# Optimization experiments

Measured on AMD Instinct MI355X. Metric: run time of the kernel, lower is better.

The kernel has to match this reference:

```python
import jax, jax.numpy as jnp
import numpy as np
from jax import lax

H = 16        # linear_num_key_heads == linear_num_value_heads
DK = 64       # linear_key_head_dim
DV = 128      # linear_value_head_dim
HID = 2048    # hidden_size
KCONV = 4     # linear_conv_kernel_dim
SEQ = 2048
KEY_DIM = H * DK       # 1024
VAL_DIM = H * DV       # 2048
CONV_DIM = 2 * KEY_DIM + VAL_DIM  # 4096


def _l2norm(x, eps=1e-6):
    return x * lax.rsqrt(jnp.sum(x * x, axis=-1, keepdims=True) + eps)


def setup_inputs() -> dict:
    key = jax.random.key(0)
    ks = jax.random.split(key, 10)
    s = 0.02
    return {
        "hidden_states": jax.random.normal(ks[0], (1, SEQ, HID), jnp.float32),
        "in_proj_qkv": jax.random.normal(ks[1], (CONV_DIM, HID), jnp.float32) * s,
        "in_proj_a": jax.random.normal(ks[2], (H, HID), jnp.float32) * s,
        "in_proj_b": jax.random.normal(ks[3], (H, HID), jnp.float32) * s,
        "in_proj_z": jax.random.normal(ks[4], (VAL_DIM, HID), jnp.float32) * s,
        "conv_w": jax.random.normal(ks[5], (CONV_DIM, 1, KCONV), jnp.float32) * 0.5,
        "A_log": jax.random.normal(ks[6], (H,), jnp.float32) * 0.5,
        "dt_bias": jnp.ones((H,), jnp.float32),
        "norm_w": jnp.ones((DV,), jnp.float32),
        "out_proj": jax.random.normal(ks[7], (HID, VAL_DIM), jnp.float32) * s,
        "is_prefill": 1,
    }


def reference(hidden_states, in_proj_qkv, in_proj_a, in_proj_b, in_proj_z,
              conv_w, A_log, dt_bias, norm_w, out_proj, is_prefill):
    b, s, _ = hidden_states.shape  # b == 1
    # QKV projection: (1, S, CONV_DIM)
    mixed = jnp.einsum('bsh,oh->bso', hidden_states, in_proj_qkv)
    # Depthwise causal conv1d over time (left pad K-1), then SiLU
    x = mixed.transpose(0, 2, 1)  # (1, C, S)
    x = lax.conv_general_dilated(
        x, conv_w, window_strides=(1,), padding=[(KCONV - 1, 0)],
        feature_group_count=CONV_DIM, dimension_numbers=('NCH', 'OIH', 'NCH'))
    mixed = jax.nn.silu(x).transpose(0, 2, 1)[0]  # (S, CONV_DIM), squeeze batch

    q = mixed[:, :KEY_DIM].reshape(s, H, DK)
    k = mixed[:, KEY_DIM:2 * KEY_DIM].reshape(s, H, DK)
    v = mixed[:, 2 * KEY_DIM:].reshape(s, H, DV)

    hs = hidden_states[0]  # (S, HID)
    a = hs @ in_proj_a.T                      # (S, H)
    g = -jnp.exp(A_log) * jax.nn.softplus(a + dt_bias)  # (S, H) log-decay
    beta = jax.nn.sigmoid(hs @ in_proj_b.T)   # (S, H)
    z = (hs @ in_proj_z.T).reshape(s, H, DV)  # (S, H, DV)

    q = _l2norm(q) * (1.0 / np.sqrt(DK))
    k = _l2norm(k)

    # Delta-rule recurrence; prefill -> zero initial state
    S0 = jnp.zeros((H, DK, DV), jnp.float32)

    def step(St, inp):
        q_t, k_t, v_t, g_t, beta_t = inp
        St = St * jnp.exp(g_t)[:, None, None]            # decay
        kv_mem = jnp.einsum('hk,hkv->hv', k_t, St)       # read
        delta = (v_t - kv_mem) * beta_t[:, None]         # gated error
        St = St + jnp.einsum('hk,hv->hkv', k_t, delta)   # rank-1 update
        o_t = jnp.einsum('hk,hkv->hv', q_t, St)          # query read
        return St, o_t

    _, core = lax.scan(step, S0, (q, k, v, g, beta))  # core: (S, H, DV)

    # Gated RMSNorm over DV, then SiLU(z) gate
    var = jnp.mean(core * core, axis=-1, keepdims=True)
    core = core * lax.rsqrt(var + 1e-6) * norm_w
    core = core * jax.nn.silu(z)
    core = core.reshape(1, s, VAL_DIM)
    return jnp.einsum('bsv,hv->bsh', core, out_proj)
```

## Files before the change

### kernel.cpp

```cpp
#include <hip/hip_runtime.h>
#include <stdint.h>


#define SEQ 2048
#define HIDDEN 2048
#define NH 16
#define DKv 64
#define DVv 128
#define KEY_DIM 1024
#define VAL_DIM 2048
#define CONV_DIM 4096

typedef __bf16 bf16;
typedef unsigned short u16;
typedef __attribute__((ext_vector_type(8))) __bf16 bf16x8;
typedef __attribute__((ext_vector_type(4))) __bf16 bf16x4;
typedef __attribute__((ext_vector_type(4))) float f32x4;

#define AS1 __attribute__((address_space(1)))
#define AS3 __attribute__((address_space(3)))
#define GLDS16(src, dst) __builtin_amdgcn_global_load_lds((AS1 const void*)(src), (AS3 void*)(dst), 16, 0, 0)

__device__ __forceinline__ float b2f(u16 u) {
  union { unsigned int i; float f; } c; c.i = ((unsigned int)u) << 16; return c.f;
}
__device__ __forceinline__ float sigmoidf_(float x) { return 1.0f / (1.0f + __expf(-x)); }

__global__ void detect_dtype(const u16* __restrict__ p, unsigned* __restrict__ flag) {
  int lane = threadIdx.x;
  int cnt = 0;
  for (int w = lane; w < 2048; w += 64) {
    unsigned e = (p[2 * w] >> 7) & 0xFF;
    if (e < 64) cnt++;
  }
  cnt += __shfl_xor(cnt, 1);  cnt += __shfl_xor(cnt, 2);  cnt += __shfl_xor(cnt, 4);
  cnt += __shfl_xor(cnt, 8);  cnt += __shfl_xor(cnt, 16); cnt += __shfl_xor(cnt, 32);
  if (lane == 0) *flag = (cnt > 64) ? 1u : 0u;
}

__global__ __launch_bounds__(256)
void cvt_bf16(const void* __restrict__ src, bf16* __restrict__ dst, long n,
              const unsigned* __restrict__ flagp) {
  long i = ((long)blockIdx.x * 256 + threadIdx.x) * 8;
  if (i >= n) return;
  if (*flagp) {
    const f32x4* s = (const f32x4*)((const float*)src + i);
    f32x4 a = s[0], b = s[1];
    bf16x8 o;
#pragma unroll
    for (int j = 0; j < 4; ++j) { o[j] = (bf16)a[j]; o[4 + j] = (bf16)b[j]; }
    *(bf16x8*)(dst + i) = o;
  } else {
    *(bf16x8*)(dst + i) = *(const bf16x8*)((const bf16*)src + i);
  }
}

template<bool F32OUT>
__global__ __launch_bounds__(256, 2)
void gemm_nt(const void* __restrict__ Araw, const void* __restrict__ Braw,
             void* __restrict__ Cv, int N, int K,
             const unsigned* __restrict__ flagp, int useA, int useB) {
  __shared__ __align__(16) bf16 As[128 * 32];
  __shared__ __align__(16) bf16 Bs[128 * 32];
  const bool f32g = (*flagp != 0);
  const bool fA = useA && f32g;
  const bool fB = useB && f32g;
  const int tid  = threadIdx.x;
  const int lane = tid & 63;
  const int wv   = tid >> 6;
  const int wm   = (wv & 1) << 6;
  const int wn   = (wv >> 1) << 6;
  const long bm  = (long)blockIdx.y * 128;
  const long bn  = (long)blockIdx.x * 128;

  f32x4 acc[4][4] = {};

  for (int k0 = 0; k0 < K; k0 += 32) {
#pragma unroll
    for (int it = 0; it < 2; ++it) {
      int e   = (it * 256 + tid) * 8;
      int row = e >> 5;
      int col = e & 31;
      long offA = (bm + row) * (long)K + (k0 + col);
      long offB = (bn + row) * (long)K + (k0 + col);
      if (fA) {
        const float* g = (const float*)Araw + offA;
        f32x4 u0 = *(const f32x4*)g, u1 = *(const f32x4*)(g + 4);
        bf16x8 bv;
#pragma unroll
        for (int j = 0; j < 4; ++j) { bv[j] = (bf16)u0[j]; bv[4 + j] = (bf16)u1[j]; }
        *(bf16x8*)&As[e] = bv;
      } else {
        const bf16* g = (const bf16*)Araw + offA;
        GLDS16(g, &As[e]);
      }
      if (fB) {
        const float* g = (const float*)Braw + offB;
        f32x4 u0 = *(const f32x4*)g, u1 = *(const f32x4*)(g + 4);
        bf16x8 bv;
#pragma unroll
        for (int j = 0; j < 4; ++j) { bv[j] = (bf16)u0[j]; bv[4 + j] = (bf16)u1[j]; }
        *(bf16x8*)&Bs[e] = bv;
      } else {
        const bf16* g = (const bf16*)Braw + offB;
        GLDS16(g, &Bs[e]);
      }
    }
    __syncthreads();

    const bf16x8* As8 = (const bf16x8*)As;
    const bf16x8* Bs8 = (const bf16x8*)Bs;
    const int r = lane & 15, q = lane >> 4;
    bf16x8 af[4], bfr[4];
#pragma unroll
    for (int i = 0; i < 4; ++i) af[i]  = As8[(wm + i * 16 + r) * 4 + q];
#pragma unroll
    for (int j = 0; j < 4; ++j) bfr[j] = Bs8[(wn + j * 16 + r) * 4 + q];
#pragma unroll
    for (int i = 0; i < 4; ++i)
#pragma unroll
      for (int j = 0; j < 4; ++j)
        acc[i][j] = __builtin_amdgcn_mfma_f32_16x16x32_bf16(af[i], bfr[j], acc[i][j], 0, 0, 0);
    __syncthreads();
  }

  const int r = lane & 15, q = lane >> 4;
#pragma unroll
  for (int i = 0; i < 4; ++i)
#pragma unroll
    for (int j = 0; j < 4; ++j) {
      long row = bm + wm + i * 16 + q * 4;
      long col = bn + wn + j * 16 + r;
#pragma unroll
      for (int rr = 0; rr < 4; ++rr) {
        if constexpr (F32OUT) ((float*)Cv)[(row + rr) * N + col] = acc[i][j][rr];
        else                  ((bf16*)Cv)[(row + rr) * N + col] = (bf16)acc[i][j][rr];
      }
    }
}

__device__ void gemm_body_bf16(char* smemc, const bf16* __restrict__ A,
                               const bf16* __restrict__ B, bf16* __restrict__ C,
                               int N, int K, int bx, int by, int tid) {
  bf16* As = (bf16*)smemc;
  bf16* Bs = (bf16*)(smemc + 8192);
  const int lane = tid & 63;
  const int wv = tid >> 6, wm = (wv & 1) << 6, wn = (wv >> 1) << 6;
  const long bm = (long)by * 128, bn = (long)bx * 128;
  f32x4 acc[4][4] = {};
  for (int k0 = 0; k0 < K; k0 += 32) {
#pragma unroll
    for (int it = 0; it < 2; ++it) {
      int e = (it * 256 + tid) * 8;
      int row = e >> 5, col = e & 31;
      const bf16* gA = A + (bm + row) * (long)K + k0 + col;
      const bf16* gB = B + (bn + row) * (long)K + k0 + col;
      GLDS16(gA, &As[e]);
      GLDS16(gB, &Bs[e]);
    }
    __syncthreads();
    const bf16x8* As8 = (const bf16x8*)As;
    const bf16x8* Bs8 = (const bf16x8*)Bs;
    const int r = lane & 15, q = lane >> 4;
    bf16x8 af[4], bfr[4];
#pragma unroll
    for (int i = 0; i < 4; ++i) af[i]  = As8[(wm + i * 16 + r) * 4 + q];
#pragma unroll
    for (int j = 0; j < 4; ++j) bfr[j] = Bs8[(wn + j * 16 + r) * 4 + q];
#pragma unroll
    for (int i = 0; i < 4; ++i)
#pragma unroll
      for (int j = 0; j < 4; ++j)
        acc[i][j] = __builtin_amdgcn_mfma_f32_16x16x32_bf16(af[i], bfr[j], acc[i][j], 0, 0, 0);
    __syncthreads();
  }
  const int r = lane & 15, q = lane >> 4;
#pragma unroll
  for (int i = 0; i < 4; ++i)
#pragma unroll
    for (int j = 0; j < 4; ++j) {
      long row = bm + wm + i * 16 + q * 4;
      long col = bn + wn + j * 16 + r;
#pragma unroll
      for (int rr = 0; rr < 4; ++rr)
        C[(row + rr) * (long)N + col] = (bf16)acc[i][j][rr];
    }
}

__global__ __launch_bounds__(256)
void proj_ab(const void* __restrict__ hsr, const void* __restrict__ War,
             const void* __restrict__ Wbr, const void* __restrict__ A_logr,
             const void* __restrict__ dtbr,
             float* __restrict__ eg, float* __restrict__ bet,
             float* __restrict__ gb,
             const unsigned* __restrict__ flagp) {
  const bool f32g = (*flagp != 0);
  const int t  = threadIdx.x;
  const int sl = t >> 5;
  const int o  = t & 31;
  const int h  = o & 15;
  const long s = (long)blockIdx.x * 8 + sl;
  float a0 = 0.f, a1 = 0.f, a2 = 0.f, a3 = 0.f;
  if (f32g) {
    const f32x4* x4 = (const f32x4*)((const float*)hsr + s * HIDDEN);
    const f32x4* w4 = (const f32x4*)((const float*)((o < 16) ? War : Wbr) + (long)h * HIDDEN);
#pragma unroll 8
    for (int k4 = 0; k4 < 512; ++k4) {
      f32x4 xv = x4[k4], wv = w4[k4];
      a0 = fmaf(xv[0], wv[0], a0);
      a1 = fmaf(xv[1], wv[1], a1);
      a2 = fmaf(xv[2], wv[2], a2);
      a3 = fmaf(xv[3], wv[3], a3);
    }
  } else {
    const bf16x8* x8 = (const bf16x8*)((const bf16*)hsr + s * HIDDEN);
    const bf16x8* w8 = (const bf16x8*)((const bf16*)((o < 16) ? War : Wbr) + (long)h * HIDDEN);
#pragma unroll 8
    for (int k8 = 0; k8 < 256; ++k8) {
      bf16x8 xv = x8[k8], wv = w8[k8];
      a0 += (float)xv[0] * (float)wv[0] + (float)xv[4] * (float)wv[4];
      a1 += (float)xv[1] * (float)wv[1] + (float)xv[5] * (float)wv[5];
      a2 += (float)xv[2] * (float)wv[2] + (float)xv[6] * (float)wv[6];
      a3 += (float)xv[3] * (float)wv[3] + (float)xv[7] * (float)wv[7];
    }
  }
  const float a = (a0 + a1) + (a2 + a3);
  if (o < 16) {
    float alog = f32g ? ((const float*)A_logr)[h] : b2f(((const u16*)A_logr)[h]);
    float dtb  = f32g ? ((const float*)dtbr)[h]   : b2f(((const u16*)dtbr)[h]);
    float xx = a + dtb;
    float sp = fmaxf(xx, 0.f) + log1pf(__expf(-fabsf(xx)));
    float gg = -__expf(alog) * sp;
    if (gb) gb[s * NH + h] = gg;
    eg[s * NH + h] = __expf(gg);
  } else {
    bet[s * NH + h] = sigmoidf_(a);
  }
}

__global__ __launch_bounds__(256)
void conv_norm(const bf16* __restrict__ mixed, const void* __restrict__ convwr,
               bf16* __restrict__ qbuf, bf16* __restrict__ kbuf, bf16* __restrict__ vbuf,
               const unsigned* __restrict__ flagp) {
  const bool f32g = (*flagp != 0);
  const int s = blockIdx.x;
  const int c = blockIdx.y * 256 + threadIdx.x;
  float w0, w1, w2, w3;
  if (f32g) {
    const float* wp = (const float*)convwr + (long)c * 4;
    w0 = wp[0]; w1 = wp[1]; w2 = wp[2]; w3 = wp[3];
  } else {
    const u16* wp = (const u16*)convwr + (long)c * 4;
    w0 = b2f(wp[0]); w1 = b2f(wp[1]); w2 = b2f(wp[2]); w3 = b2f(wp[3]);
  }
  float acc = w3 * (float)mixed[(long)s * CONV_DIM + c];
  if (s >= 1) acc += w2 * (float)mixed[(long)(s - 1) * CONV_DIM + c];
  if (s >= 2) acc += w1 * (float)mixed[(long)(s - 2) * CONV_DIM + c];
  if (s >= 3) acc += w0 * (float)mixed[(long)(s - 3) * CONV_DIM + c];
  float y = acc * sigmoidf_(acc);
  if (c < 2 * KEY_DIM) {
    float ss = y * y;
    ss += __shfl_xor(ss, 1);  ss += __shfl_xor(ss, 2);  ss += __shfl_xor(ss, 4);
    ss += __shfl_xor(ss, 8);  ss += __shfl_xor(ss, 16); ss += __shfl_xor(ss, 32);
    float scale = rsqrtf(ss + 1e-6f);
    if (c < KEY_DIM) scale *= 0.125f;
    y *= scale;
  }
  if (c < KEY_DIM)            qbuf[(long)s * KEY_DIM + c] = (bf16)y;
  else if (c < 2 * KEY_DIM)   kbuf[(long)s * KEY_DIM + (c - KEY_DIM)] = (bf16)y;
  else                        vbuf[(long)s * VAL_DIM + (c - 2 * KEY_DIM)] = (bf16)y;
}

template<int CTRL>
__device__ __forceinline__ float dpp_add(float x) {
  int y = __builtin_amdgcn_update_dpp(0, __float_as_int(x), CTRL, 0xF, 0xF, true);
  return x + __int_as_float(y);
}
__device__ __forceinline__ float dpp_sum16(float x) {
  x = dpp_add<0xB1>(x);
  x = dpp_add<0x4E>(x);
  x = dpp_add<0x141>(x);
  x = dpp_add<0x140>(x);
  return x;
}

__global__ __launch_bounds__(256, 2)
void fused_scan(const bf16* __restrict__ qbuf, const bf16* __restrict__ kbuf,
                const bf16* __restrict__ vbuf, const float* __restrict__ eg,
                const float* __restrict__ bet, bf16* __restrict__ core,
                const bf16* __restrict__ hsb, const bf16* __restrict__ wzb,
                bf16* __restrict__ zbuf, const void* __restrict__ woutr,
                bf16* __restrict__ woutb, const unsigned* __restrict__ flagp,
                int nScan, int nGemm) {
  __shared__ __align__(16) char smem[16384];
  const int t = threadIdx.x;
  const int b = blockIdx.x;

  if (b < nScan) {
    const int h  = b >> 3;
    const int vg = (b & 7) * 16;
    const int g  = t >> 4;
    const int L  = t & 15;
    bf16*  kqs = (bf16*)smem;
    bf16*  vts = (bf16*)(smem + 8192);
    float* ets = (float*)(smem + 9216);
    float* bts = (float*)(smem + 9344);

#define STAGE(buf, s0)                                                          \
    {                                                                           \
      int byte = t * 16;                                                        \
      const bf16* src;                                                          \
      if (byte < 2048) {                                                        \
        int row = byte >> 7, el = (byte & 127) >> 1;                            \
        src = kbuf + (long)((s0) + row) * KEY_DIM + h * DKv + el;               \
      } else {                                                                  \
        int b2 = byte - 2048;                                                   \
        int row = b2 >> 7, el = (b2 & 127) >> 1;                                \
        src = qbuf + (long)((s0) + row) * KEY_DIM + h * DKv + el;               \
      }                                                                         \
      GLDS16(src, smem + (buf) * 4096 + byte);                                  \
      if (t < 32) {                                                             \
        int row = t >> 1, el = (t & 1) * 8;                                     \
        const bf16* vsrc = vbuf + (long)((s0) + row) * VAL_DIM + h * DVv + vg + el; \
        GLDS16(vsrc, smem + 8192 + (buf) * 512 + t * 16);                       \
      }                                                                         \
    }

    float er = 0.f, br = 0.f;
    if (t < 16)      er = eg[(long)t * NH + h];
    else if (t < 32) br = bet[(long)(t - 16) * NH + h];
    STAGE(0, 0);
    if (t < 16)      ets[t] = er;
    else if (t < 32) bts[t - 16] = br;
    __syncthreads();

    float S0 = 0.f, S1 = 0.f, S2 = 0.f, S3 = 0.f;
    for (int tile = 0; tile < 128; ++tile) {
      const int buf = tile & 1, nb = buf ^ 1;
      if (tile < 127) {
        STAGE(nb, (tile + 1) * 16);
        if (t < 16)      er = eg[(long)((tile + 1) * 16 + t) * NH + h];
        else if (t < 32) br = bet[(long)((tile + 1) * 16 + (t - 16)) * NH + h];
      }
      const bf16*  ktb = kqs + buf * 2048;
      const bf16*  qtb = ktb + 1024;
      const bf16*  vtb = vts + buf * 256;
      const float* etb = ets + buf * 16;
      const float* btb = bts + buf * 16;
      const long sbase = (long)tile * 16;

      bf16x4 kR[2], qR[2];
      float  vR[2], eR[2], bR[2];
      kR[0] = *(const bf16x4*)(ktb + 0 * 64 + L * 4);
      qR[0] = *(const bf16x4*)(qtb + 0 * 64 + L * 4);
      vR[0] = (float)vtb[0 * 16 + g];  eR[0] = etb[0];  bR[0] = btb[0];
      kR[1] = *(const bf16x4*)(ktb + 1 * 64 + L * 4);
      qR[1] = *(const bf16x4*)(qtb + 1 * 64 + L * 4);
      vR[1] = (float)vtb[1 * 16 + g];  eR[1] = etb[1];  bR[1] = btb[1];
#pragma unroll
      for (int s = 0; s < 16; ++s) {
        const int sl = s & 1;
        bf16x4 kk = kR[sl], qq = qR[sl];
        float vv = vR[sl], ee = eR[sl], bb = bR[sl];
        if (s < 14) {
          const int s2 = s + 2;
          kR[sl] = *(const bf16x4*)(ktb + s2 * 64 + L * 4);
          qR[sl] = *(const bf16x4*)(qtb + s2 * 64 + L * 4);
          vR[sl] = (float)vtb[s2 * 16 + g];
          eR[sl] = etb[s2];  bR[sl] = btb[s2];
        }
        float ebt = ee * bb, vbt = vv * bb;
        float k0 = (float)kk[0], k1 = (float)kk[1], k2 = (float)kk[2], k3 = (float)kk[3];
        float D0 = S0 * ee, D1 = S1 * ee, D2 = S2 * ee, D3 = S3 * ee;
        float p = (k0 * S0 + k1 * S1) + (k2 * S2 + k3 * S3);
        p = dpp_sum16(p);
        float delta = vbt - ebt * p;
        S0 = fmaf(k0, delta, D0); S1 = fmaf(k1, delta, D1);
        S2 = fmaf(k2, delta, D2); S3 = fmaf(k3, delta, D3);
        float q0 = (float)qq[0], q1 = (float)qq[1], q2 = (float)qq[2], q3 = (float)qq[3];
        float o = (q0 * S0 + q1 * S1) + (q2 * S2 + q3 * S3);
        o = dpp_sum16(o);
        if (L == 0) core[(sbase + s) * VAL_DIM + h * DVv + vg + g] = (bf16)o;
      }
      if (tile < 127) {
        if (t < 16)      ets[nb * 16 + t] = er;
        else if (t < 32) bts[nb * 16 + (t - 16)] = br;
      }
      __syncthreads();
    }
#undef STAGE
  } else if (b < nScan + nGemm) {
    int gb = b - nScan;
    gemm_body_bf16(smem, hsb, wzb, zbuf, VAL_DIM, HIDDEN, gb & 15, gb >> 4, t);
  } else {
    long i = ((long)(b - nScan - nGemm) * 256 + t) * 8;
    if (i < (long)HIDDEN * VAL_DIM) {
      if (*flagp) {
        const f32x4* s = (const f32x4*)((const float*)woutr + i);
        f32x4 a = s[0], c = s[1];
        bf16x8 o;
#pragma unroll
        for (int j = 0; j < 4; ++j) { o[j] = (bf16)a[j]; o[4 + j] = (bf16)c[j]; }
        *(bf16x8*)(woutb + i) = o;
      } else {
        *(bf16x8*)(woutb + i) = *(const bf16x8*)((const bf16*)woutr + i);
      }
    }
  }
}


__global__ __launch_bounds__(256, 2)
void chunk_a(const bf16* __restrict__ kbuf, const bf16* __restrict__ vbuf,
             const float* __restrict__ gbuf, const float* __restrict__ betp,
             bf16* __restrict__ dloc, bf16* __restrict__ whig, bf16* __restrict__ wlog,
             const bf16* __restrict__ hsb, const bf16* __restrict__ wzb,
             bf16* __restrict__ zbuf, const void* __restrict__ woutr,
             bf16* __restrict__ woutb, const unsigned* __restrict__ flagp) {
  __shared__ __align__(16) char smem[25600];
  const int t = threadIdx.x;
  const int b = blockIdx.x;
  if (b < 512) {
    const int c = b >> 4, h = b & 15;
    bf16*  Ks   = (bf16*)smem;
    float* At   = (float*)(smem + 8192);
    float* cumS = (float*)(smem + 24576);
    float* bS   = (float*)(smem + 24832);
    float* dS   = (float*)(smem + 25088);
#pragma unroll
    for (int it = 0; it < 2; ++it) {
      int byte = (it * 256 + t) * 16;
      int row = byte >> 7, col = (byte & 127) >> 1;
      const bf16* src = kbuf + (long)(c * 64 + row) * KEY_DIM + h * DKv + col;
      GLDS16(src, smem + byte);
    }
    if (t < 64) {
      float cc = gbuf[(long)(c * 64 + t) * NH + h];
#pragma unroll
      for (int d = 1; d < 64; d <<= 1) { float y = __shfl_up(cc, d); if (t >= d) cc += y; }
      cumS[t] = cc;
      dS[t] = __expf(cc);
      bS[t] = betp[(long)(c * 64 + t) * NH + h];
    }
    {
      f32x4 z = {0.f, 0.f, 0.f, 0.f};
#pragma unroll
      for (int i = 0; i < 4; ++i) ((f32x4*)At)[t * 4 + i] = z;
    }
    __syncthreads();
    {
      const int lane = t & 63, wv = t >> 6;
      const int r = lane & 15, q = lane >> 4;
      const bf16x8* Ks8 = (const bf16x8*)Ks;
#pragma unroll
      for (int n = 0; n < 4; ++n) {
        f32x4 acc = {0.f, 0.f, 0.f, 0.f};
#pragma unroll
        for (int kk = 0; kk < 2; ++kk) {
          bf16x8 af  = Ks8[(wv * 16 + r) * 8 + kk * 4 + q];
          bf16x8 bfv = Ks8[(n  * 16 + r) * 8 + kk * 4 + q];
          acc = __builtin_amdgcn_mfma_f32_16x16x32_bf16(af, bfv, acc, 0, 0, 0);
        }
        const int i = n * 16 + r;
#pragma unroll
        for (int rr = 0; rr < 4; ++rr) {
          const int tr = wv * 16 + q * 4 + rr;
          if (i < tr)
            At[i * 64 + tr] = bS[tr] * __expf(cumS[tr] - cumS[i]) * acc[rr];
        }
      }
    }
    __syncthreads();
    if (t < 192) {
      float x[64];
      const long base = ((long)(c * 16 + h)) * 64;
      if (t < 128) {
#pragma unroll
        for (int s = 0; s < 64; ++s)
          x[s] = bS[s] * (float)vbuf[(long)(c * 64 + s) * VAL_DIM + h * DVv + t];
      } else {
        const int k = t - 128;
#pragma unroll
        for (int s = 0; s < 64; ++s)
          x[s] = bS[s] * dS[s] * (float)Ks[s * 64 + k];
      }
#pragma unroll
      for (int s = 0; s < 64; ++s) {
        const float val = x[s];
        const f32x4* row4 = (const f32x4*)(At + s * 64);
#pragma unroll
        for (int qd = (s >> 2); qd < 16; ++qd) {
          f32x4 a4 = row4[qd];
          x[qd * 4 + 0] = fmaf(-a4[0], val, x[qd * 4 + 0]);
          x[qd * 4 + 1] = fmaf(-a4[1], val, x[qd * 4 + 1]);
          x[qd * 4 + 2] = fmaf(-a4[2], val, x[qd * 4 + 2]);
          x[qd * 4 + 3] = fmaf(-a4[3], val, x[qd * 4 + 3]);
        }
      }
      if (t < 128) {
#pragma unroll
        for (int s = 0; s < 64; ++s)
          dloc[(base + s) * 128 + t] = (bf16)x[s];
      } else {
        const int k = t - 128;
        const long wb = base * 64;
#pragma unroll
        for (int s = 0; s < 64; ++s) {
          float v = -x[s];
          bf16 hh = (bf16)v;
          whig[wb + s * 64 + k] = hh;
          wlog[wb + s * 64 + k] = (bf16)(v - (float)hh);
        }
      }
    }
  } else if (b < 768) {
    int gb = b - 512;
    gemm_body_bf16(smem, hsb, wzb, zbuf, VAL_DIM, HIDDEN, gb & 15, gb >> 4, t);
  } else {
    long i = ((long)(b - 768) * 256 + t) * 8;
    if (i < (long)HIDDEN * VAL_DIM) {
      if (*flagp) {
        const f32x4* s = (const f32x4*)((const float*)woutr + i);
        f32x4 a = s[0], cc = s[1];
        bf16x8 o;
#pragma unroll
        for (int j = 0; j < 4; ++j) { o[j] = (bf16)a[j]; o[4 + j] = (bf16)cc[j]; }
        *(bf16x8*)(woutb + i) = o;
      } else {
        *(bf16x8*)(woutb + i) = *(const bf16x8*)((const bf16*)woutr + i);
      }
    }
  }
}

__global__ __launch_bounds__(256, 1)
void chunk_b(const bf16* __restrict__ qbuf, const bf16* __restrict__ kbuf,
             const float* __restrict__ gbuf, const bf16* __restrict__ dloc,
             const bf16* __restrict__ whig, const bf16* __restrict__ wlog,
             bf16* __restrict__ dTg, bf16* __restrict__ o1g) {
  __shared__ __align__(16) char smem[139264];
  bf16* Wh  = (bf16*)(smem);
  bf16* Wl  = (bf16*)(smem + 16384);
  bf16* Qs  = (bf16*)(smem + 32768);
  bf16* Ks  = (bf16*)(smem + 49152);
  bf16* Dls = (bf16*)(smem + 65536);
  bf16* KT  = (bf16*)(smem + 81920);
  bf16* Shi = (bf16*)(smem + 90112);
  bf16* Slo = (bf16*)(smem + 98304);
  bf16* Dth = (bf16*)(smem + 106496);
  bf16* Dtl = (bf16*)(smem + 114688);
  float* fSa = (float*)(smem + 122880);
  float* dSa = (float*)(smem + 131072);

  const int t = threadIdx.x;
  const int h = blockIdx.x >> 1, vhalf = blockIdx.x & 1;
  const int lane = t & 63, w = t >> 6;
  const int r = lane & 15, q = lane >> 4;
  const int tb = w * 16 + q * 4;

  auto stage = [&](int bb, int cc) {
    const long c16h = (long)(cc * 16 + h);
#pragma unroll
    for (int it = 0; it < 2; ++it) {
      int p = it * 256 + t;
      int row = p >> 3, g = p & 7;
      int sg = ((g ^ (row & 7)) << 3);
      GLDS16(whig + c16h * 4096 + row * 64 + sg, (char*)Wh + bb * 8192 + p * 16);
      GLDS16(wlog + c16h * 4096 + row * 64 + sg, (char*)Wl + bb * 8192 + p * 16);
      GLDS16(qbuf + (long)(cc * 64 + row) * KEY_DIM + h * DKv + sg, (char*)Qs + bb * 8192 + p * 16);
      GLDS16(kbuf + (long)(cc * 64 + row) * KEY_DIM + h * DKv + (g << 3), (char*)Ks + bb * 8192 + p * 16);
      GLDS16(dloc + (c16h * 64 + row) * 128 + vhalf * 64 + sg, (char*)Dls + bb * 8192 + p * 16);
    }
  };

  {
    float g8[8];
#pragma unroll
    for (int i = 0; i < 8; ++i)
      g8[i] = gbuf[(long)((w * 8 + i) * 64 + lane) * NH + h];
#pragma unroll
    for (int i = 0; i < 8; ++i) {
      float cs = g8[i];
#pragma unroll
      for (int d = 1; d < 64; d <<= 1) { float y = __shfl_up(cs, d); if (lane >= d) cs += y; }
      float tot = __shfl(cs, 63);
      fSa[(w * 8 + i) * 64 + lane] = __expf(tot - cs);
      dSa[(w * 8 + i) * 64 + lane] = __expf(cs);
    }
  }
  {
    f32x4 z = {0.f, 0.f, 0.f, 0.f};
    ((f32x4*)Shi)[t] = z; ((f32x4*)Shi)[t + 256] = z;
    ((f32x4*)Slo)[t] = z; ((f32x4*)Slo)[t + 256] = z;
  }
  stage(0, 0);
  f32x4 Sacc[4] = {};

  for (int c = 0; c < 32; ++c) {
    const int buf = c & 1, nb = buf ^ 1;
    __syncthreads();
    if (c < 31) stage(nb, c + 1);
    const bf16* wh = Wh + buf * 4096;
    const bf16* wl = Wl + buf * 4096;
    const bf16* qs = Qs + buf * 4096;
    const bf16* ks = Ks + buf * 4096;
    const bf16* dl = Dls + buf * 4096;
    const float* fS = fSa + c * 64;
    const float* dS = dSa + c * 64;
    const long gch = (long)(c * 16 + h) * 8192 + (long)(vhalf * 64) * 64;

    if (c < 31) {
      const int k = lane;
#pragma unroll
      for (int ii = 0; ii < 16; ++ii) {
        const int i = w * 16 + ii;
        const int pg = (i >> 3) ^ (k & 7);
        KT[k * 64 + pg * 8 + (i & 7)] = ks[i * 64 + k];
      }
    }

    float fs4[4], ds4[4];
#pragma unroll
    for (int rr = 0; rr < 4; ++rr) { fs4[rr] = fS[tb + rr]; ds4[rr] = dS[tb + rr]; }

    bf16x8 wahi[2], walo[2], qa[2];
#pragma unroll
    for (int kk = 0; kk < 2; ++kk) {
      const int row = w * 16 + r;
      const int g = (kk * 4 + q) ^ (row & 7);
      wahi[kk] = *(const bf16x8*)(wh + row * 64 + g * 8);
      walo[kk] = *(const bf16x8*)(wl + row * 64 + g * 8);
      qa[kk]   = *(const bf16x8*)(qs + row * 64 + g * 8);
    }
    bf16x8 sh[4][2], sl[4][2];
#pragma unroll
    for (int n = 0; n < 4; ++n)
#pragma unroll
      for (int kk = 0; kk < 2; ++kk) {
        const int vrow = n * 16 + r;
        const int g = (kk * 4 + q) ^ (vrow & 7);
        sh[n][kk] = *(const bf16x8*)(Shi + vrow * 64 + g * 8);
        sl[n][kk] = *(const bf16x8*)(Slo + vrow * 64 + g * 8);
      }
    float dl4[4][4];
#pragma unroll
    for (int n = 0; n < 4; ++n)
#pragma unroll
      for (int rr = 0; rr < 4; ++rr) {
        const int vrow = n * 16 + r, trow = tb + rr;
        const int pg = (vrow >> 3) ^ (trow & 7);
        dl4[n][rr] = (float)dl[trow * 64 + pg * 8 + (vrow & 7)];
      }

    f32x4 da[4] = {}, oa[4] = {};
#pragma unroll
    for (int n = 0; n < 4; ++n)
#pragma unroll
      for (int kk = 0; kk < 2; ++kk) {
        da[n] = __builtin_amdgcn_mfma_f32_16x16x32_bf16(wahi[kk], sh[n][kk], da[n], 0, 0, 0);
        da[n] = __builtin_amdgcn_mfma_f32_16x16x32_bf16(wahi[kk], sl[n][kk], da[n], 0, 0, 0);
        da[n] = __builtin_amdgcn_mfma_f32_16x16x32_bf16(walo[kk], sh[n][kk], da[n], 0, 0, 0);
        oa[n] = __builtin_amdgcn_mfma_f32_16x16x32_bf16(qa[kk],   sh[n][kk], oa[n], 0, 0, 0);
        oa[n] = __builtin_amdgcn_mfma_f32_16x16x32_bf16(qa[kk],   sl[n][kk], oa[n], 0, 0, 0);
      }

#pragma unroll
    for (int n = 0; n < 4; ++n) {
      const int vrow = n * 16 + r;
      bf16x4 dpk, opk, fhk, flk;
#pragma unroll
      for (int rr = 0; rr < 4; ++rr) {
        float dv = dl4[n][rr] + da[n][rr];
        dpk[rr] = (bf16)dv;
        float p = fs4[rr] * dv;
        bf16 ph = (bf16)p;
        fhk[rr] = ph;
        flk[rr] = (bf16)(p - (float)ph);
        opk[rr] = (bf16)(ds4[rr] * oa[n][rr]);
      }
      *(bf16x4*)(dTg + gch + (long)vrow * 64 + tb) = dpk;
      *(bf16x4*)(o1g + gch + (long)vrow * 64 + tb) = opk;
      const int pg = (tb >> 3) ^ (vrow & 7);
      *(bf16x4*)(Dth + vrow * 64 + pg * 8 + (tb & 7)) = fhk;
      *(bf16x4*)(Dtl + vrow * 64 + pg * 8 + (tb & 7)) = flk;
    }

    __syncthreads();
    if (c < 31) {
      const float dC = dS[63];
      bf16x8 dh[2], dlo2[2], ktf[4][2];
#pragma unroll
      for (int kk = 0; kk < 2; ++kk) {
        const int vrow = w * 16 + r;
        const int g = (kk * 4 + q) ^ (vrow & 7);
        dh[kk]   = *(const bf16x8*)(Dth + vrow * 64 + g * 8);
        dlo2[kk] = *(const bf16x8*)(Dtl + vrow * 64 + g * 8);
      }
#pragma unroll
      for (int n = 0; n < 4; ++n)
#pragma unroll
        for (int kk = 0; kk < 2; ++kk) {
          const int krow = n * 16 + r;
          const int g = (kk * 4 + q) ^ (krow & 7);
          ktf[n][kk] = *(const bf16x8*)(KT + krow * 64 + g * 8);
        }
#pragma unroll
      for (int n = 0; n < 4; ++n) {
        f32x4 sa;
#pragma unroll
        for (int rr = 0; rr < 4; ++rr) sa[rr] = dC * Sacc[n][rr];
#pragma unroll
        for (int kk = 0; kk < 2; ++kk) {
          sa = __builtin_amdgcn_mfma_f32_16x16x32_bf16(dh[kk],   ktf[n][kk], sa, 0, 0, 0);
          sa = __builtin_amdgcn_mfma_f32_16x16x32_bf16(dlo2[kk], ktf[n][kk], sa, 0, 0, 0);
        }
        Sacc[n] = sa;
        const int k = n * 16 + r;
#pragma unroll
        for (int rr = 0; rr < 4; ++rr) {
          const int v = tb + rr;
          float s = sa[rr];
          bf16 hh = (bf16)s;
          const int pg = (k >> 3) ^ (v & 7);
          Shi[v * 64 + pg * 8 + (k & 7)] = hh;
          Slo[v * 64 + pg * 8 + (k & 7)] = (bf16)(s - (float)hh);
        }
      }
    }
  }
}

__global__ __launch_bounds__(256, 2)
void chunk_c(const bf16* __restrict__ qbuf, const bf16* __restrict__ kbuf,
             const float* __restrict__ gbuf, const bf16* __restrict__ dTg,
             const bf16* __restrict__ o1g, bf16* __restrict__ core) {
  __shared__ __align__(16) char smem[57600];
  const int t = threadIdx.x;
  const int c = blockIdx.x >> 4, h = blockIdx.x & 15;
  const long c16h = (long)(c * 16 + h);
  bf16* Qs  = (bf16*)smem;
  bf16* Ksl = (bf16*)(smem + 8192);
  bf16* Pl  = (bf16*)(smem + 16384);
  const bf16* dT  = (const bf16*)(smem + 24576);
  const bf16* o1l = (const bf16*)(smem + 40960);
  float* cumS = (float*)(smem + 57344);

#pragma unroll
  for (int it = 0; it < 2; ++it) {
    int byte = (it * 256 + t) * 16;
    int row = byte >> 7, col = (byte & 127) >> 1;
    GLDS16(qbuf + (long)(c * 64 + row) * KEY_DIM + h * DKv + col, smem + byte);
    GLDS16(kbuf + (long)(c * 64 + row) * KEY_DIM + h * DKv + col, smem + 8192 + byte);
  }
#pragma unroll
  for (int it = 0; it < 4; ++it) {
    int byte = (it * 256 + t) * 16;
    GLDS16(dTg + c16h * 8192 + (byte >> 1), smem + 24576 + byte);
    GLDS16(o1g + c16h * 8192 + (byte >> 1), smem + 40960 + byte);
  }
  if (t < 64) {
    float cc = gbuf[(long)(c * 64 + t) * NH + h];
#pragma unroll
    for (int d = 1; d < 64; d <<= 1) { float y = __shfl_up(cc, d); if (t >= d) cc += y; }
    cumS[t] = cc;
  }
  __syncthreads();

  const int lane = t & 63, wv = t >> 6;
  const int r = lane & 15, q = lane >> 4;
  const bf16x8* Qs8 = (const bf16x8*)Qs;
  const bf16x8* Ks8 = (const bf16x8*)Ksl;

#pragma unroll
  for (int n = 0; n < 4; ++n) {
    f32x4 acc = {0.f, 0.f, 0.f, 0.f};
#pragma unroll
    for (int kk = 0; kk < 2; ++kk)
      acc = __builtin_amdgcn_mfma_f32_16x16x32_bf16(
          Qs8[(wv * 16 + r) * 8 + kk * 4 + q], Ks8[(n * 16 + r) * 8 + kk * 4 + q], acc, 0, 0, 0);
    const int i = n * 16 + r;
#pragma unroll
    for (int rr = 0; rr < 4; ++rr) {
      const int tr = wv * 16 + q * 4 + rr;
      Pl[tr * 64 + i] = (i <= tr) ? (bf16)(__expf(cumS[tr] - cumS[i]) * acc[rr]) : (bf16)0.0f;
    }
  }
  __syncthreads();

  {
    const bf16x8* Pl8 = (const bf16x8*)Pl;
    const bf16x8* dT8 = (const bf16x8*)dT;
    bf16x8 pf[2];
#pragma unroll
    for (int kk = 0; kk < 2; ++kk) pf[kk] = Pl8[(wv * 16 + r) * 8 + kk * 4 + q];
#pragma unroll
    for (int n = 0; n < 8; ++n) {
      const int v = n * 16 + r;
      f32x4 acc;
#pragma unroll
      for (int rr = 0; rr < 4; ++rr)
        acc[rr] = (float)o1l[v * 64 + (wv * 16 + q * 4 + rr)];
#pragma unroll
      for (int kk = 0; kk < 2; ++kk)
        acc = __builtin_amdgcn_mfma_f32_16x16x32_bf16(
            pf[kk], dT8[(n * 16 + r) * 8 + kk * 4 + q], acc, 0, 0, 0);
#pragma unroll
      for (int rr = 0; rr < 4; ++rr) {
        const int tr = wv * 16 + q * 4 + rr;
        core[(long)(c * 64 + tr) * VAL_DIM + h * DVv + v] = (bf16)acc[rr];
      }
    }
  }
}

__global__ __launch_bounds__(256)
void gate_norm(const bf16* __restrict__ core, const bf16* __restrict__ zb,
               const void* __restrict__ normwr, bf16* __restrict__ gated,
               const unsigned* __restrict__ flagp) {
  const bool f32g = (*flagp != 0);
  const int s  = blockIdx.x;
  const int t  = threadIdx.x;
  const int h  = t >> 4;
  const int li = t & 15;
  const long base = (long)s * VAL_DIM + h * DVv + li * 8;
  bf16x8 c8 = *(const bf16x8*)(core + base);
  bf16x8 z8 = *(const bf16x8*)(zb + base);
  float x[8], z[8], nw[8];
  float ss = 0.f;
#pragma unroll
  for (int j = 0; j < 8; ++j) { x[j] = (float)c8[j]; z[j] = (float)z8[j]; ss += x[j] * x[j]; }
  if (f32g) {
    const float* np_ = (const float*)normwr + li * 8;
#pragma unroll
    for (int j = 0; j < 8; ++j) nw[j] = np_[j];
  } else {
    const u16* np_ = (const u16*)normwr + li * 8;
#pragma unroll
    for (int j = 0; j < 8; ++j) nw[j] = b2f(np_[j]);
  }
  ss += __shfl_xor(ss, 1); ss += __shfl_xor(ss, 2);
  ss += __shfl_xor(ss, 4); ss += __shfl_xor(ss, 8);
  float scale = rsqrtf(ss * (1.f / 128.f) + 1e-6f);
#pragma unroll
  for (int j = 0; j < 8; ++j) {
    float y = x[j] * scale * nw[j];
    y *= z[j] * sigmoidf_(z[j]);
    gated[base + j] = (bf16)y;
  }
}

extern "C" void kernel_launch(void* const* d_in, const int* in_sizes, int n_in,
                              void* d_out, int out_size, void* d_ws, size_t ws_size,
                              hipStream_t stream) {
  char* ws = (char*)d_ws;
  const bool big = ws_size >= ((48u << 20) + (512u << 10));

  if (big) {
    bf16*  hsb   = (bf16*)ws;
    bf16*  wqkvb = (bf16*)(ws + (8u << 20));
    bf16*  wzb   = (bf16*)(ws + (8u << 20));
    bf16*  zbuf  = (bf16*)(ws + (16u << 20));
    bf16*  mixed = (bf16*)(ws + (24u << 20));
    bf16*  whig  = (bf16*)(ws + (24u << 20));
    bf16*  wlog  = (bf16*)(ws + (28u << 20));
    bf16*  woutb = (bf16*)(ws + (32u << 20));
    bf16*  qbuf  = (bf16*)(ws + (40u << 20));
    bf16*  kbuf  = (bf16*)(ws + (44u << 20));
    bf16*  gated = (bf16*)(ws + (40u << 20));
    bf16*  dTg   = (bf16*)ws;
    bf16*  o1g   = (bf16*)(ws + (8u << 20));
    float* egp  = (float*)(ws + (48u << 20));
    float* betp = (float*)(ws + (48u << 20) + (128u << 10));
    float* gbp  = (float*)(ws + (48u << 20) + (256u << 10));
    unsigned* flagp = (unsigned*)(ws + (48u << 20) + (384u << 10));
    bf16* vbuf  = (bf16*)d_out;
    bf16* dlocp = (bf16*)((char*)d_out + (8u << 20));
    bf16* corep = (bf16*)d_out;

    detect_dtype<<<1, 64, 0, stream>>>((const u16*)d_in[0], flagp);
    proj_ab<<<SEQ / 8, 256, 0, stream>>>(d_in[0], d_in[2], d_in[3], d_in[6], d_in[7], egp, betp, gbp, flagp);
    cvt_bf16<<<(SEQ * HIDDEN) / 2048, 256, 0, stream>>>(d_in[0], hsb, (long)SEQ * HIDDEN, flagp);
    cvt_bf16<<<(CONV_DIM * HIDDEN) / 2048, 256, 0, stream>>>(d_in[1], wqkvb, (long)CONV_DIM * HIDDEN, flagp);
    gemm_nt<false><<<dim3(CONV_DIM / 128, SEQ / 128), 256, 0, stream>>>(hsb, wqkvb, mixed, CONV_DIM, HIDDEN, flagp, 0, 0);
    cvt_bf16<<<(VAL_DIM * HIDDEN) / 2048, 256, 0, stream>>>(d_in[4], wzb, (long)VAL_DIM * HIDDEN, flagp);
    conv_norm<<<dim3(SEQ, CONV_DIM / 256), 256, 0, stream>>>(mixed, d_in[5], qbuf, kbuf, vbuf, flagp);
    chunk_a<<<512 + 256 + 2048, 256, 0, stream>>>(kbuf, vbuf, gbp, betp, dlocp, whig, wlog,
                                                  hsb, wzb, zbuf, d_in[9], woutb, flagp);
    chunk_b<<<32, 256, 0, stream>>>(qbuf, kbuf, gbp, dlocp, whig, wlog, dTg, o1g);
    chunk_c<<<512, 256, 0, stream>>>(qbuf, kbuf, gbp, dTg, o1g, corep);
    gate_norm<<<SEQ, 256, 0, stream>>>(corep, zbuf, d_in[8], gated, flagp);
    gemm_nt<true><<<dim3(HIDDEN / 128, SEQ / 128), 256, 0, stream>>>(gated, woutb, d_out, HIDDEN, VAL_DIM, flagp, 0, 0);
  } else {
    bf16* mixed = (bf16*)ws;
    bf16* qbuf  = (bf16*)(ws + (16u << 20));
    bf16* kbuf  = (bf16*)(ws + (20u << 20));
    bf16* zbuf  = (bf16*)ws;
    bf16* corep = (bf16*)(ws + (8u << 20));
    bf16* gated = (bf16*)(ws + (16u << 20));
    float* egp  = (float*)(ws + (24u << 20));
    float* betp = (float*)(ws + (24u << 20) + (128u << 10));
    unsigned* flagp = (unsigned*)(ws + (24u << 20) + (256u << 10));
    bf16* vbuf  = (bf16*)d_out;

    detect_dtype<<<1, 64, 0, stream>>>((const u16*)d_in[0], flagp);
    proj_ab<<<SEQ / 8, 256, 0, stream>>>(d_in[0], d_in[2], d_in[3], d_in[6], d_in[7], egp, betp, nullptr, flagp);
    gemm_nt<false><<<dim3(CONV_DIM / 128, SEQ / 128), 256, 0, stream>>>(d_in[0], d_in[1], mixed, CONV_DIM, HIDDEN, flagp, 1, 1);
    conv_norm<<<dim3(SEQ, CONV_DIM / 256), 256, 0, stream>>>(mixed, d_in[5], qbuf, kbuf, vbuf, flagp);
    gemm_nt<false><<<dim3(VAL_DIM / 128, SEQ / 128), 256, 0, stream>>>(d_in[0], d_in[4], zbuf, VAL_DIM, HIDDEN, flagp, 1, 1);
    fused_scan<<<128, 256, 0, stream>>>(qbuf, kbuf, vbuf, egp, betp, corep,
                                        nullptr, nullptr, nullptr, nullptr, nullptr, flagp,
                                        128, 0);
    gate_norm<<<SEQ, 256, 0, stream>>>(corep, zbuf, d_in[8], gated, flagp);
    gemm_nt<true><<<dim3(HIDDEN / 128, SEQ / 128), 256, 0, stream>>>(gated, d_in[9], d_out, HIDDEN, VAL_DIM, flagp, 0, 1);
  }
}
```

Measured before the change: 491.1 us.

## Split chunk_b recurrence across four value-quarter blocks per head

The sequential inter-chunk state recurrence kernel now runs 64 blocks (four value quarters per head) instead of 32, so each block carries a 32x64 state slice and less LDS. chunk_a writes the local delta values transposed (per v row, contiguous over time) with vectorized stores, so chunk_b can stage its quarter with a single async load and read four values at once. The state update work is redistributed across waves, and the end-of-chunk __syncthreads is replaced by an explicit lgkmcnt wait plus s_barrier. The aim is to shorten the serial critical path by using more CUs, at the cost of duplicated W/Q/K loads and KT transposes per block.

```diff
diff --git a/kernel.cpp b/kernel.cpp
--- a/kernel.cpp
+++ b/kernel.cpp
@@ -413,7 +413,7 @@
 __global__ __launch_bounds__(256, 2)
 void chunk_a(const bf16* __restrict__ kbuf, const bf16* __restrict__ vbuf,
              const float* __restrict__ gbuf, const float* __restrict__ betp,
-             bf16* __restrict__ dloc, bf16* __restrict__ whig, bf16* __restrict__ wlog,
+             bf16* __restrict__ dlocT, bf16* __restrict__ whig, bf16* __restrict__ wlog,
              const bf16* __restrict__ hsb, const bf16* __restrict__ wzb,
              bf16* __restrict__ zbuf, const void* __restrict__ woutr,
              bf16* __restrict__ woutb, const unsigned* __restrict__ flagp) {
@@ -473,7 +473,7 @@
     __syncthreads();
     if (t < 192) {
       float x[64];
-      const long base = ((long)(c * 16 + h)) * 64;
+      const long ch = (long)(c * 16 + h);
       if (t < 128) {
 #pragma unroll
         for (int s = 0; s < 64; ++s)
@@ -498,12 +498,17 @@
         }
       }
       if (t < 128) {
-#pragma unroll
-        for (int s = 0; s < 64; ++s)
-          dloc[(base + s) * 128 + t] = (bf16)x[s];
+        bf16* dp = dlocT + ch * 8192 + (long)t * 64;
+#pragma unroll
+        for (int s4 = 0; s4 < 16; ++s4) {
+          bf16x4 o;
+          o[0] = (bf16)x[s4 * 4 + 0]; o[1] = (bf16)x[s4 * 4 + 1];
+          o[2] = (bf16)x[s4 * 4 + 2]; o[3] = (bf16)x[s4 * 4 + 3];
+          *(bf16x4*)(dp + s4 * 4) = o;
+        }
       } else {
         const int k = t - 128;
-        const long wb = base * 64;
+        const long wb = ch * 4096;
 #pragma unroll
         for (int s = 0; s < 64; ++s) {
           float v = -x[s];
@@ -535,25 +540,25 @@
 
 __global__ __launch_bounds__(256, 1)
 void chunk_b(const bf16* __restrict__ qbuf, const bf16* __restrict__ kbuf,
-             const float* __restrict__ gbuf, const bf16* __restrict__ dloc,
+             const float* __restrict__ gbuf, const bf16* __restrict__ dlocT,
              const bf16* __restrict__ whig, const bf16* __restrict__ wlog,
              bf16* __restrict__ dTg, bf16* __restrict__ o1g) {
-  __shared__ __align__(16) char smem[139264];
+  __shared__ __align__(16) char smem[114688];
   bf16* Wh  = (bf16*)(smem);
   bf16* Wl  = (bf16*)(smem + 16384);
   bf16* Qs  = (bf16*)(smem + 32768);
   bf16* Ks  = (bf16*)(smem + 49152);
   bf16* Dls = (bf16*)(smem + 65536);
-  bf16* KT  = (bf16*)(smem + 81920);
-  bf16* Shi = (bf16*)(smem + 90112);
-  bf16* Slo = (bf16*)(smem + 98304);
-  bf16* Dth = (bf16*)(smem + 106496);
-  bf16* Dtl = (bf16*)(smem + 114688);
-  float* fSa = (float*)(smem + 122880);
-  float* dSa = (float*)(smem + 131072);
+  bf16* KT  = (bf16*)(smem + 73728);
+  bf16* Shi = (bf16*)(smem + 81920);
+  bf16* Slo = (bf16*)(smem + 86016);
+  bf16* Dth = (bf16*)(smem + 90112);
+  bf16* Dtl = (bf16*)(smem + 94208);
+  float* fSa = (float*)(smem + 98304);
+  float* dSa = (float*)(smem + 106496);
 
   const int t = threadIdx.x;
-  const int h = blockIdx.x >> 1, vhalf = blockIdx.x & 1;
+  const int h = blockIdx.x >> 2, vq = blockIdx.x & 3;
   const int lane = t & 63, w = t >> 6;
   const int r = lane & 15, q = lane >> 4;
   const int tb = w * 16 + q * 4;
@@ -569,7 +574,12 @@
       GLDS16(wlog + c16h * 4096 + row * 64 + sg, (char*)Wl + bb * 8192 + p * 16);
       GLDS16(qbuf + (long)(cc * 64 + row) * KEY_DIM + h * DKv + sg, (char*)Qs + bb * 8192 + p * 16);
       GLDS16(kbuf + (long)(cc * 64 + row) * KEY_DIM + h * DKv + (g << 3), (char*)Ks + bb * 8192 + p * 16);
-      GLDS16(dloc + (c16h * 64 + row) * 128 + vhalf * 64 + sg, (char*)Dls + bb * 8192 + p * 16);
+    }
+    {
+      int row = t >> 3, g = t & 7;
+      int sg = ((g ^ (row & 7)) << 3);
+      GLDS16(dlocT + c16h * 8192 + (long)(vq * 32 + row) * 64 + sg,
+             (char*)Dls + bb * 4096 + t * 16);
     }
   };
 
@@ -590,11 +600,13 @@
   }
   {
     f32x4 z = {0.f, 0.f, 0.f, 0.f};
-    ((f32x4*)Shi)[t] = z; ((f32x4*)Shi)[t + 256] = z;
-    ((f32x4*)Slo)[t] = z; ((f32x4*)Slo)[t + 256] = z;
+    ((f32x4*)Shi)[t] = z;
+    ((f32x4*)Slo)[t] = z;
   }
   stage(0, 0);
-  f32x4 Sacc[4] = {};
+  f32x4 Sacc[2] = {};
+
+  const int va = w & 1, kt0 = (w >> 1) * 2;
 
   for (int c = 0; c < 32; ++c) {
     const int buf = c & 1, nb = buf ^ 1;
@@ -604,18 +616,18 @@
     const bf16* wl = Wl + buf * 4096;
     const bf16* qs = Qs + buf * 4096;
     const bf16* ks = Ks + buf * 4096;
-    const bf16* dl = Dls + buf * 4096;
+    const bf16* dls = Dls + buf * 2048;
     const float* fS = fSa + c * 64;
     const float* dS = dSa + c * 64;
-    const long gch = (long)(c * 16 + h) * 8192 + (long)(vhalf * 64) * 64;
+    const long gch = (long)(c * 16 + h) * 8192 + (long)(vq * 32) * 64;
 
     if (c < 31) {
-      const int k = lane;
+      const int k2 = lane;
 #pragma unroll
       for (int ii = 0; ii < 16; ++ii) {
         const int i = w * 16 + ii;
-        const int pg = (i >> 3) ^ (k & 7);
-        KT[k * 64 + pg * 8 + (i & 7)] = ks[i * 64 + k];
+        const int pg = (i >> 3) ^ (k2 & 7);
+        KT[k2 * 64 + pg * 8 + (i & 7)] = ks[i * 64 + k2];
       }
     }
 
@@ -632,9 +644,9 @@
       walo[kk] = *(const bf16x8*)(wl + row * 64 + g * 8);
       qa[kk]   = *(const bf16x8*)(qs + row * 64 + g * 8);
     }
-    bf16x8 sh[4][2], sl[4][2];
-#pragma unroll
-    for (int n = 0; n < 4; ++n)
+    bf16x8 sh[2][2], sl[2][2];
+#pragma unroll
+    for (int n = 0; n < 2; ++n)
 #pragma unroll
       for (int kk = 0; kk < 2; ++kk) {
         const int vrow = n * 16 + r;
@@ -642,19 +654,19 @@
         sh[n][kk] = *(const bf16x8*)(Shi + vrow * 64 + g * 8);
         sl[n][kk] = *(const bf16x8*)(Slo + vrow * 64 + g * 8);
       }
-    float dl4[4][4];
-#pragma unroll
-    for (int n = 0; n < 4; ++n)
-#pragma unroll
-      for (int rr = 0; rr < 4; ++rr) {
-        const int vrow = n * 16 + r, trow = tb + rr;
-        const int pg = (vrow >> 3) ^ (trow & 7);
-        dl4[n][rr] = (float)dl[trow * 64 + pg * 8 + (vrow & 7)];
-      }
-
-    f32x4 da[4] = {}, oa[4] = {};
-#pragma unroll
-    for (int n = 0; n < 4; ++n)
+    float dl4[2][4];
+#pragma unroll
+    for (int n = 0; n < 2; ++n) {
+      const int vloc = n * 16 + r;
+      const int pg = (tb >> 3) ^ (vloc & 7);
+      bf16x4 dv4 = *(const bf16x4*)(dls + vloc * 64 + pg * 8 + (tb & 7));
+#pragma unroll
+      for (int rr = 0; rr < 4; ++rr) dl4[n][rr] = (float)dv4[rr];
+    }
+
+    f32x4 da[2] = {}, oa[2] = {};
+#pragma unroll
+    for (int n = 0; n < 2; ++n)
 #pragma unroll
       for (int kk = 0; kk < 2; ++kk) {
         da[n] = __builtin_amdgcn_mfma_f32_16x16x32_bf16(wahi[kk], sh[n][kk], da[n], 0, 0, 0);
@@ -665,8 +677,8 @@
       }
 
 #pragma unroll
-    for (int n = 0; n < 4; ++n) {
-      const int vrow = n * 16 + r;
+    for (int n = 0; n < 2; ++n) {
+      const int vloc = n * 16 + r;
       bf16x4 dpk, opk, fhk, flk;
 #pragma unroll
       for (int rr = 0; rr < 4; ++rr) {
@@ -678,47 +690,51 @@
         flk[rr] = (bf16)(p - (float)ph);
         opk[rr] = (bf16)(ds4[rr] * oa[n][rr]);
       }
-      *(bf16x4*)(dTg + gch + (long)vrow * 64 + tb) = dpk;
-      *(bf16x4*)(o1g + gch + (long)vrow * 64 + tb) = opk;
-      const int pg = (tb >> 3) ^ (vrow & 7);
-      *(bf16x4*)(Dth + vrow * 64 + pg * 8 + (tb & 7)) = fhk;
-      *(bf16x4*)(Dtl + vrow * 64 + pg * 8 + (tb & 7)) = flk;
-    }
-
-    __syncthreads();
+      *(bf16x4*)(dTg + gch + (long)vloc * 64 + tb) = dpk;
+      *(bf16x4*)(o1g + gch + (long)vloc * 64 + tb) = opk;
+      const int pg = (tb >> 3) ^ (vloc & 7);
+      *(bf16x4*)(Dth + vloc * 64 + pg * 8 + (tb & 7)) = fhk;
+      *(bf16x4*)(Dtl + vloc * 64 + pg * 8 + (tb & 7)) = flk;
+    }
+
+    asm volatile("s_waitcnt lgkmcnt(0)" ::: "memory");
+    __builtin_amdgcn_sched_barrier(0);
+    __builtin_amdgcn_s_barrier();
+    __builtin_amdgcn_sched_barrier(0);
+
     if (c < 31) {
       const float dC = dS[63];
-      bf16x8 dh[2], dlo2[2], ktf[4][2];
+      bf16x8 dh[2], dlo2[2], ktf[2][2];
 #pragma unroll
       for (int kk = 0; kk < 2; ++kk) {
-        const int vrow = w * 16 + r;
+        const int vrow = va * 16 + r;
         const int g = (kk * 4 + q) ^ (vrow & 7);
         dh[kk]   = *(const bf16x8*)(Dth + vrow * 64 + g * 8);
         dlo2[kk] = *(const bf16x8*)(Dtl + vrow * 64 + g * 8);
       }
 #pragma unroll
-      for (int n = 0; n < 4; ++n)
+      for (int m = 0; m < 2; ++m)
 #pragma unroll
         for (int kk = 0; kk < 2; ++kk) {
-          const int krow = n * 16 + r;
+          const int krow = (kt0 + m) * 16 + r;
           const int g = (kk * 4 + q) ^ (krow & 7);
-          ktf[n][kk] = *(const bf16x8*)(KT + krow * 64 + g * 8);
+          ktf[m][kk] = *(const bf16x8*)(KT + krow * 64 + g * 8);
         }
 #pragma unroll
-      for (int n = 0; n < 4; ++n) {
+      for (int m = 0; m < 2; ++m) {
         f32x4 sa;
 #pragma unroll
-        for (int rr = 0; rr < 4; ++rr) sa[rr] = dC * Sacc[n][rr];
+        for (int rr = 0; rr < 4; ++rr) sa[rr] = dC * Sacc[m][rr];
 #pragma unroll
         for (int kk = 0; kk < 2; ++kk) {
-          sa = __builtin_amdgcn_mfma_f32_16x16x32_bf16(dh[kk],   ktf[n][kk], sa, 0, 0, 0);
-          sa = __builtin_amdgcn_mfma_f32_16x16x32_bf16(dlo2[kk], ktf[n][kk], sa, 0, 0, 0);
+          sa = __builtin_amdgcn_mfma_f32_16x16x32_bf16(dh[kk],   ktf[m][kk], sa, 0, 0, 0);
+          sa = __builtin_amdgcn_mfma_f32_16x16x32_bf16(dlo2[kk], ktf[m][kk], sa, 0, 0, 0);
         }
-        Sacc[n] = sa;
-        const int k = n * 16 + r;
+        Sacc[m] = sa;
+        const int k = (kt0 + m) * 16 + r;
 #pragma unroll
         for (int rr = 0; rr < 4; ++rr) {
-          const int v = tb + rr;
+          const int v = va * 16 + q * 4 + rr;
           float s = sa[rr];
           bf16 hh = (bf16)s;
           const int pg = (k >> 3) ^ (v & 7);
@@ -886,7 +902,7 @@
     conv_norm<<<dim3(SEQ, CONV_DIM / 256), 256, 0, stream>>>(mixed, d_in[5], qbuf, kbuf, vbuf, flagp);
     chunk_a<<<512 + 256 + 2048, 256, 0, stream>>>(kbuf, vbuf, gbp, betp, dlocp, whig, wlog,
                                                   hsb, wzb, zbuf, d_in[9], woutb, flagp);
-    chunk_b<<<32, 256, 0, stream>>>(qbuf, kbuf, gbp, dlocp, whig, wlog, dTg, o1g);
+    chunk_b<<<64, 256, 0, stream>>>(qbuf, kbuf, gbp, dlocp, whig, wlog, dTg, o1g);
     chunk_c<<<512, 256, 0, stream>>>(qbuf, kbuf, gbp, dTg, o1g, corep);
     gate_norm<<<SEQ, 256, 0, stream>>>(corep, zbuf, d_in[8], gated, flagp);
     gemm_nt<true><<<dim3(HIDDEN / 128, SEQ / 128), 256, 0, stream>>>(gated, woutb, d_out, HIDDEN, VAL_DIM, flagp, 0, 0);
```

Result: no change. 499.2 us (+1.6%).
